# Kernel tuning notes

Measured on AMD Instinct MI355X. Metric: run time of the kernel, lower is better.

The kernel has to match this reference:

```python
import jax, jax.numpy as jnp
import numpy as np

QA = 4  # quaternion dimension (qa in the torch code)


def _bingham_sample(lam, key):
    """ACG rejection sampler for Bingham(lam), lam > 0, shape [N, 4].
    Faithful to bingham_rj: resample rejected rows until all accepted.
    Implemented with a fixed-shape lax.while_loop (resample everything,
    keep accepted rows via where) so it is jit-compatible."""
    sigacginv = 1.0 + 2.0 * lam            # [N,4]
    sig = jnp.sqrt(1.0 / sigacginv)        # SigACG, per-component std
    N = lam.shape[0]
    X0 = jnp.zeros((N, QA), lam.dtype)
    acc0 = jnp.zeros((N,), dtype=bool)

    half_qa = QA / 2.0
    log_qa = jnp.log(jnp.asarray(QA, lam.dtype))

    def cond(state):
        _, acc, _ = state
        return ~jnp.all(acc)

    def body(state):
        X, acc, key = state
        key, k1, k2 = jax.random.split(key, 3)
        yp = jax.random.normal(k1, (N, QA), lam.dtype) * sig
        y = yp / jnp.linalg.norm(yp, axis=1, keepdims=True)
        y2 = y * y
        lratio = (-jnp.sum(y2 * lam, axis=1)
                  - half_qa * log_qa
                  + 0.5 * (QA - 1)
                  + half_qa * jnp.log(jnp.sum(y2 * sigacginv, axis=1)))
        u = jax.random.uniform(k2, (N,), lam.dtype)
        # torch code: X[indx] = y (overwrite not-yet-accepted), then decide accept
        X = jnp.where(acc[:, None], X, y)
        acc = acc | (jnp.log(u) < lratio)
        return X, acc, key

    X, _, _ = jax.lax.while_loop(cond, body, (X0, acc0, key))
    return X


def _make_E(qn):
    """Build z_Q [N,4,4] from unit quaternions, exactly as reparameterize_rj."""
    q0, q1, q2, q3 = qn[:, 0], qn[:, 1], qn[:, 2], qn[:, 3]
    r1 = jnp.stack([q0, -q1, -q2, q3], axis=-1)
    r2 = jnp.stack([q1, q0, q3, q2], axis=-1)
    r3 = jnp.stack([q2, -q3, q0, -q1], axis=-1)
    r4 = jnp.stack([q3, q2, -q1, -q0], axis=-1)
    return jnp.stack([r1, r2, r3, r4], axis=1)  # rows stacked along dim 1


def setup_inputs() -> dict:
    key = jax.random.key(0)
    kq, kz = jax.random.split(key)
    N = 1048576
    q = jax.random.normal(kq, (N, 4), jnp.float32)
    # strictly negative, monotonically decreasing concentrations (Z0<Z1<Z2 in |.|)
    dZ = jax.random.uniform(kz, (N, 3), jnp.float32, minval=1e-3, maxval=100.0)
    Zbatch = -jnp.cumsum(dZ, axis=1)  # [N,3], all < 0
    return {"q": q, "Zbatch": Zbatch, "seed": 42}


def reference(q, Zbatch, seed):
    # F.normalize on the quaternion output (done in forward before reparameterize_rj)
    qn = q / jnp.linalg.norm(q, axis=1, keepdims=True)
    E = _make_E(qn)                                              # [N,4,4]
    N = q.shape[0]
    Zexp = jnp.concatenate(
        [jnp.full((N, 1), -1e-6, Zbatch.dtype), Zbatch], axis=1)  # [N,4], all < 0
    lam = -Zexp                                                   # lam > 0
    X = _bingham_sample(lam, jax.random.key(seed))                # [N,4]
    # torch.bmm(E.transpose(1,2), X.unsqueeze(2)).squeeze() == E^T @ x per row
    return jnp.einsum('nij,ni->nj', E, X)
```

## Files before the change

### kernel.cpp

```cpp
#include <hip/hip_runtime.h>
#include <cstdint>


#define DEVI __device__ __forceinline__
#define MAXT 96
#define GRID 512
#define NT 256
#define CMAX 2048
#define GANGA 56
#define NG 16
#define GW 4

DEVI uint32_t rotl32(uint32_t v, int s) { return (v << s) | (v >> (32 - s)); }

DEVI void tf2x32(uint32_t k0, uint32_t k1, uint32_t x0, uint32_t x1,
                 uint32_t& o0, uint32_t& o1) {
  const uint32_t kx = k0 ^ k1 ^ 0x1BD11BDAu;
  x0 += k0; x1 += k1;
#define TFR(r) x0 += x1; x1 = rotl32(x1, (r)); x1 ^= x0;
  TFR(13) TFR(15) TFR(26) TFR(6)
  x0 += k1; x1 += kx + 1u;
  TFR(17) TFR(29) TFR(16) TFR(24)
  x0 += kx; x1 += k0 + 2u;
  TFR(13) TFR(15) TFR(26) TFR(6)
  x0 += k0; x1 += k1 + 3u;
  TFR(17) TFR(29) TFR(16) TFR(24)
  x0 += k1; x1 += kx + 4u;
  TFR(13) TFR(15) TFR(26) TFR(6)
  x0 += kx; x1 += k0 + 5u;
#undef TFR
  o0 = x0; o1 = x1;
}

DEVI void tf_round5(uint32_t x0[5], uint32_t x1[5], int rr) {
#pragma unroll
  for (int j = 0; j < 5; ++j) {
    x0[j] += x1[j];
    x1[j] = rotl32(x1[j], rr);
    x1[j] ^= x0[j];
  }
}
DEVI void tf_inj5(uint32_t x0[5], uint32_t x1[5],
                  const uint32_t* sa, const uint32_t* sb, uint32_t add) {
#pragma unroll
  for (int j = 0; j < 5; ++j) { x0[j] += sa[j]; x1[j] += sb[j] + add; }
}

DEVI float u01_from_bits(uint32_t bits) {
  return __fsub_rn(__uint_as_float(0x3f800000u | (bits >> 9)), 1.0f);
}

DEVI void trial5(uint4 ck, uint32_t base, uint32_t ctr, float u[5]) {
  uint32_t s0[5], s1[5], s2k[5], x0[5], x1[5];
#pragma unroll
  for (int j = 0; j < 5; ++j) {
    uint32_t k0 = (j < 4) ? ck.x : ck.z;
    uint32_t k1 = (j < 4) ? ck.y : ck.w;
    s0[j] = k0; s1[j] = k1; s2k[j] = k0 ^ k1 ^ 0x1BD11BDAu;
    uint32_t c = (j < 4) ? (base + (uint32_t)j) : ctr;
    x0[j] = k0;
    x1[j] = c + k1;
  }
  tf_round5(x0, x1, 13); tf_round5(x0, x1, 15);
  tf_round5(x0, x1, 26); tf_round5(x0, x1, 6);
  tf_inj5(x0, x1, s1, s2k, 1u);
  tf_round5(x0, x1, 17); tf_round5(x0, x1, 29);
  tf_round5(x0, x1, 16); tf_round5(x0, x1, 24);
  tf_inj5(x0, x1, s2k, s0, 2u);
  tf_round5(x0, x1, 13); tf_round5(x0, x1, 15);
  tf_round5(x0, x1, 26); tf_round5(x0, x1, 6);
  tf_inj5(x0, x1, s0, s1, 3u);
  tf_round5(x0, x1, 17); tf_round5(x0, x1, 29);
  tf_round5(x0, x1, 16); tf_round5(x0, x1, 24);
  tf_inj5(x0, x1, s1, s2k, 4u);
  tf_round5(x0, x1, 13); tf_round5(x0, x1, 15);
  tf_round5(x0, x1, 26); tf_round5(x0, x1, 6);
  tf_inj5(x0, x1, s2k, s0, 5u);
#pragma unroll
  for (int j = 0; j < 5; ++j) u[j] = u01_from_bits(x0[j] ^ x1[j]);
}

template <int K>
DEVI void xla_logf_pos_k(const float* xf, float* out) {
  float e[K], m[K], z[K], y[K];
#pragma unroll
  for (int j = 0; j < K; ++j) {
    uint32_t bits = __float_as_uint(xf[j]);
    e[j] = (float)((int)(bits >> 23) - 126);
    m[j] = __uint_as_float((bits & 0x007fffffu) | 0x3f000000u);
    bool mc = m[j] < 0.70710678118654752440f;
    float e_lo = __fsub_rn(e[j], 1.0f);
    float m_lo = __fadd_rn(__fsub_rn(m[j], 1.0f), m[j]);
    float m_hi = __fsub_rn(m[j], 1.0f);
    e[j] = mc ? e_lo : e[j];
    m[j] = mc ? m_lo : m_hi;
    z[j] = __fmul_rn(m[j], m[j]);
    y[j] = 7.0376836292e-2f;
  }
  const float LC[8] = {-1.1514610310e-1f,  1.1676998740e-1f,
                       -1.2420140846e-1f,  1.4249322787e-1f,
                       -1.6668057665e-1f,  2.0000714765e-1f,
                       -2.4999993993e-1f,  3.3333331174e-1f};
#pragma unroll
  for (int s = 0; s < 8; ++s)
#pragma unroll
    for (int j = 0; j < K; ++j)
      y[j] = __fadd_rn(__fmul_rn(y[j], m[j]), LC[s]);
#pragma unroll
  for (int j = 0; j < K; ++j) {
    float t = __fmul_rn(__fmul_rn(y[j], m[j]), z[j]);
    t = __fadd_rn(t, __fmul_rn(e[j], -2.12194440e-4f));
    t = __fsub_rn(t, __fmul_rn(z[j], 0.5f));
    float r = __fadd_rn(m[j], t);
    out[j] = __fadd_rn(r, __fmul_rn(e[j], 0.693359375f));
  }
}

DEVI void xla_erfinv4_logu(const float* xin, float uu, float* res,
                           float& lg_uu) {
  float v[4], vp1[5], big[5], w[4], q[4], p[4];
  bool c[4];
#pragma unroll
  for (int j = 0; j < 4; ++j) {
    v[j] = -__fmul_rn(xin[j], xin[j]);
    vp1[j] = __fadd_rn(v[j], 1.0f);
  }
  vp1[4] = uu;
  xla_logf_pos_k<5>(vp1, big);
  lg_uu = big[4];
#pragma unroll
  for (int j = 0; j < 4; ++j) {
    float small = __fmul_rn(__fadd_rn(__fmul_rn(-0.5f, v[j]), 1.0f), v[j]);
    float l1p = (fabsf(v[j]) < 1e-4f) ? small : big[j];
    w[j] = -l1p;
    c[j] = (w[j] < 5.0f);
    float qc = __fsub_rn(w[j], 2.5f);
    float qr = __fsub_rn(sqrtf(w[j]), 3.0f);
    q[j] = c[j] ? qc : qr;
    p[j] = c[j] ? 2.81022636e-08f : -0.000200214257f;
  }
  const float CF[8] = { 3.43273939e-07f, -3.5233877e-06f, -4.39150654e-06f,
                        0.00021858087f,  -0.00125372503f, -0.00417768164f,
                        0.246640727f,     1.50140941f};
  const float CR[8] = { 0.000100950558f,  0.00134934322f, -0.00367342844f,
                        0.00573950773f,  -0.0076224613f,   0.00943887047f,
                        1.00167406f,      2.83297682f};
#pragma unroll
  for (int s = 0; s < 8; ++s)
#pragma unroll
    for (int j = 0; j < 4; ++j)
      p[j] = __fadd_rn(__fmul_rn(p[j], q[j]), c[j] ? CF[s] : CR[s]);
#pragma unroll
  for (int j = 0; j < 4; ++j) res[j] = __fmul_rn(p[j], xin[j]);
}

DEVI bool trial_eval(uint4 ck, int r,
                     float lam1, float lam2, float lam3,
                     float sgi1, float sgi2, float sgi3,
                     float sig1, float sig2, float sig3,
                     float sgi0, float sig0,
                     float& ry0, float& ry1, float& ry2, float& ry3) {
  const uint32_t base = ((uint32_t)r) * 4u;

  float u5[5];
  trial5(ck, base, (uint32_t)r, u5);
  float uu = u5[4];

  float xin[4];
#pragma unroll
  for (int j = 0; j < 4; ++j) {
    float x = __fadd_rn(__fmul_rn(u5[j], 2.0f), -0.99999994f);
    xin[j] = fmaxf(-0.99999994f, x);
  }
  float er[4], lg_uu;
  xla_erfinv4_logu(xin, uu, er, lg_uu);

  float y0 = __fmul_rn(__fmul_rn(1.41421356237309504880f, er[0]), sig0);
  float y1 = __fmul_rn(__fmul_rn(1.41421356237309504880f, er[1]), sig1);
  float y2v = __fmul_rn(__fmul_rn(1.41421356237309504880f, er[2]), sig2);
  float y3 = __fmul_rn(__fmul_rn(1.41421356237309504880f, er[3]), sig3);

  float n2 = __fmul_rn(y0, y0);
  n2 = __fadd_rn(n2, __fmul_rn(y1, y1));
  n2 = __fadd_rn(n2, __fmul_rn(y2v, y2v));
  n2 = __fadd_rn(n2, __fmul_rn(y3, y3));
  float nr = sqrtf(n2);
  y0 = __fdiv_rn(y0, nr); y1 = __fdiv_rn(y1, nr);
  y2v = __fdiv_rn(y2v, nr); y3 = __fdiv_rn(y3, nr);

  float s0q = __fmul_rn(y0, y0), s1q = __fmul_rn(y1, y1);
  float s2q = __fmul_rn(y2v, y2v), s3q = __fmul_rn(y3, y3);

  float s1v = __fmul_rn(s0q, 1e-6f);
  s1v = __fadd_rn(s1v, __fmul_rn(s1q, lam1));
  s1v = __fadd_rn(s1v, __fmul_rn(s2q, lam2));
  s1v = __fadd_rn(s1v, __fmul_rn(s3q, lam3));

  float s2v = __fmul_rn(s0q, sgi0);
  s2v = __fadd_rn(s2v, __fmul_rn(s1q, sgi1));
  s2v = __fadd_rn(s2v, __fmul_rn(s2q, sgi2));
  s2v = __fadd_rn(s2v, __fmul_rn(s3q, sgi3));

  float lg_s2[1];
  xla_logf_pos_k<1>(&s2v, lg_s2);

  float lr = __fsub_rn(-s1v, 2.7725887298583984f);
  lr = __fadd_rn(lr, 1.5f);
  lr = __fadd_rn(lr, __fmul_rn(2.0f, lg_s2[0]));

  float lu = (uu > 0.0f) ? lg_uu : -__builtin_inff();

  ry0 = y0; ry1 = y1; ry2 = y2v; ry3 = y3;
  return (lu < lr);
}

__global__ __launch_bounds__(256, 2) void campose_kernel(
    const float* __restrict__ q, const float* __restrict__ Z,
    float* __restrict__ out, const int* __restrict__ seedp, int N, int C) {
  __shared__ uint4 chain[MAXT + 1];
  __shared__ float rc[9][CMAX];
  __shared__ uint32_t next_row;
  __shared__ uint32_t wm;

  const int tid = threadIdx.x;
  const int lane = tid & 63;
  const int rbeg = blockIdx.x * C;
  const int rend = min(N, rbeg + C);
  const int crows = rend - rbeg;
  if (tid == 0) { next_row = (uint32_t)(rbeg + 192); wm = 0u; }

  for (int i = tid; i < crows; i += NT) {
    float z0 = Z[(size_t)(rbeg + i) * 3 + 0];
    float z1 = Z[(size_t)(rbeg + i) * 3 + 1];
    float z2 = Z[(size_t)(rbeg + i) * 3 + 2];
    float l1 = -z0, l2 = -z1, l3 = -z2;
    float g1 = __fadd_rn(1.0f, __fmul_rn(2.0f, l1));
    float g2 = __fadd_rn(1.0f, __fmul_rn(2.0f, l2));
    float g3 = __fadd_rn(1.0f, __fmul_rn(2.0f, l3));
    float s1_ = sqrtf(__fdiv_rn(1.0f, g1));
    float s2_ = sqrtf(__fdiv_rn(1.0f, g2));
    float s3_ = sqrtf(__fdiv_rn(1.0f, g3));
    rc[0][i] = g1; rc[1][i] = g2; rc[2][i] = g3;
    rc[3][i] = s1_; rc[4][i] = s2_; rc[5][i] = s3_;
    rc[6][i] = l1; rc[7][i] = l2; rc[8][i] = l3;
  }
  __syncthreads();

  const int wave = tid >> 6;
  if (wave == 0) {
    uint32_t ka = 0u, kb = (uint32_t)seedp[0];
    uint32_t x1i = (lane == 2) ? 0u : (uint32_t)(lane + 1);
    for (int t = 0; t < MAXT; ++t) {
      uint32_t o0 = 0u, o1 = 0u;
      if (lane < 3) tf2x32(ka, kb, 0u, x1i, o0, o1);
      uint32_t s1a = __shfl(o0, 0, 64), s1b = __shfl(o1, 0, 64);
      uint32_t s2a = __shfl(o0, 1, 64), s2b = __shfl(o1, 1, 64);
      if (lane == 0) chain[t] = make_uint4(s1a, s1b, s2a, s2b);
      ka = __shfl(o0, 2, 64); kb = __shfl(o1, 2, 64);
      __threadfence_block();
      if (lane == 0) *(volatile uint32_t*)&wm = (uint32_t)(t + 1);
    }
    if (lane == 0) chain[MAXT] = make_uint4(0u, 0u, 0u, 0u);
    __threadfence_block();
    if (lane == 0) *(volatile uint32_t*)&wm = (uint32_t)(MAXT + 1);
  }

  const float sgi0 = __fadd_rn(1.0f, __fmul_rn(2.0f, 1e-6f));
  const float sig0 = sqrtf(__fdiv_rn(1.0f, sgi0));

  int r, rn;
  if (wave == 0) {
    r  = (int)atomicAdd(&next_row, 1u);
    rn = (int)atomicAdd(&next_row, 1u);
  } else {
    r  = rbeg + (tid - 64);
    rn = (int)atomicAdd(&next_row, 1u);
  }
  bool have = (r < rend);
  float lam1 = 0, lam2 = 0, lam3 = 0;
  float sgi1 = 1, sgi2 = 1, sgi3 = 1;
  float sig1 = 1, sig2 = 1, sig3 = 1;
  if (have) {
    int li = r - rbeg;
    sgi1 = rc[0][li]; sgi2 = rc[1][li]; sgi3 = rc[2][li];
    sig1 = rc[3][li]; sig2 = rc[4][li]; sig3 = rc[5][li];
    lam1 = rc[6][li]; lam2 = rc[7][li]; lam3 = rc[8][li];
  }

  uint32_t wml = *(volatile uint32_t*)&wm;
  while (wml < 1u) wml = *(volatile uint32_t*)&wm;
  __threadfence_block();
  const uint4 ck0 = chain[0];
  uint4 ck = ck0;
  int t = 0;

  while (true) {
    uint64_t msk = __ballot(have);
    if (__popcll(msk) <= GANGA) break;
    if (have) {
      if (wml < (uint32_t)(t + 2)) {
        uint32_t w_ = *(volatile uint32_t*)&wm;
        while (w_ < (uint32_t)(t + 2)) w_ = *(volatile uint32_t*)&wm;
        __threadfence_block();
        wml = w_;
      }
      uint4 ckn = chain[t + 1];

      float y0, y1, y2v, y3;
      bool alr = trial_eval(ck, r, lam1, lam2, lam3, sgi1, sgi2, sgi3,
                            sig1, sig2, sig3, sgi0, sig0, y0, y1, y2v, y3);

      ++t;
      if (alr || (t >= MAXT)) {
        *reinterpret_cast<float4*>(out + (size_t)r * 4) =
            make_float4(y0, y1, y2v, y3);
        r = rn;
        int li = (r < rend ? r : rend - 1) - rbeg;
        sgi1 = rc[0][li]; sgi2 = rc[1][li]; sgi3 = rc[2][li];
        sig1 = rc[3][li]; sig2 = rc[4][li]; sig3 = rc[5][li];
        lam1 = rc[6][li]; lam2 = rc[7][li]; lam3 = rc[8][li];
        t = 0;
        ck = ck0;
        have = (r < rend);
        rn = (int)atomicAdd(&next_row, 1u);
      } else {
        ck = ckn;
      }
    }
  }

  uint64_t mask = __ballot(have);
  if (mask) {
    if (wml < (uint32_t)(MAXT + 1)) {
      uint32_t w_ = *(volatile uint32_t*)&wm;
      while (w_ < (uint32_t)(MAXT + 1)) w_ = *(volatile uint32_t*)&wm;
      __threadfence_block();
      wml = w_;
    }
    while (mask) {
      int G = __popcll(mask); if (G > NG) G = NG;
      const int g = lane >> 2, k = lane & 3;
      const bool gact = (g < G);
      const int gidx = gact ? g : 0;
      uint64_t m = mask;
      int sl = __ffsll((unsigned long long)m) - 1;
#pragma unroll
      for (int i = 1; i < NG; ++i) {
        m &= m - 1;
        int b = __ffsll((unsigned long long)m) - 1;
        sl = (i <= gidx && b >= 0) ? b : sl;
      }
      int rg = __shfl(r, sl, 64);
      int tg = __shfl(t, sl, 64);
      int li = rg - rbeg;
      float G1 = rc[0][li], G2 = rc[1][li], G3 = rc[2][li];
      float S1 = rc[3][li], S2 = rc[4][li], S3 = rc[5][li];
      float L1 = rc[6][li], L2 = rc[7][li], L3 = rc[8][li];
      int ts = tg + k;
      int tsc = ts < (MAXT - 1) ? ts : (MAXT - 1);
      uint4 cks = chain[tsc];
      float y0, y1, y2v, y3;
      bool alr = trial_eval(cks, rg, L1, L2, L3, G1, G2, G3,
                            S1, S2, S3, sgi0, sig0, y0, y1, y2v, y3);
      bool acc = alr || (ts >= MAXT - 1);
      uint64_t bal = __ballot(acc && gact);
      uint64_t gb = (bal >> (g * GW)) & 0xfull;
      int kwin = gb ? (__ffsll((unsigned long long)gb) - 1) : GW;
      if (gact && k == kwin) {
        *reinterpret_cast<float4*>(out + (size_t)rg * 4) =
            make_float4(y0, y1, y2v, y3);
      }
      int myidx = __popcll(mask & ((1ull << lane) - 1ull));
      if (have && myidx < G) {
        uint64_t gbb = (bal >> (myidx * GW)) & 0xfull;
        if (gbb) {
          r = rn;
          t = 0;
          have = (r < rend);
          rn = (int)atomicAdd(&next_row, 1u);
        } else {
          t += GW;
        }
      }
      mask = __ballot(have);
    }
  }

  __syncthreads();
  for (int i = rbeg + tid; i < rend; i += NT) {
    float4 yv = *reinterpret_cast<const float4*>(out + (size_t)i * 4);
    float4 qv = *reinterpret_cast<const float4*>(q + (size_t)i * 4);
    float a = qv.x, b = qv.y, c = qv.z, d = qv.w;
    float qn2 = __fmul_rn(a, a);
    qn2 = __fadd_rn(qn2, __fmul_rn(b, b));
    qn2 = __fadd_rn(qn2, __fmul_rn(c, c));
    qn2 = __fadd_rn(qn2, __fmul_rn(d, d));
    float qnr = sqrtf(qn2);
    a = __fdiv_rn(a, qnr); b = __fdiv_rn(b, qnr);
    c = __fdiv_rn(c, qnr); d = __fdiv_rn(d, qnr);
    float y0 = yv.x, y1 = yv.y, y2v = yv.z, y3 = yv.w;
    float o0v = __fadd_rn(__fadd_rn(__fadd_rn(__fmul_rn(a, y0), __fmul_rn(b, y1)),
                                    __fmul_rn(c, y2v)), __fmul_rn(d, y3));
    float o1v = __fadd_rn(__fadd_rn(__fadd_rn(__fmul_rn(-b, y0), __fmul_rn(a, y1)),
                                    __fmul_rn(-d, y2v)), __fmul_rn(c, y3));
    float o2v = __fadd_rn(__fadd_rn(__fadd_rn(__fmul_rn(-c, y0), __fmul_rn(d, y1)),
                                    __fmul_rn(a, y2v)), __fmul_rn(-b, y3));
    float o3v = __fadd_rn(__fadd_rn(__fadd_rn(__fmul_rn(d, y0), __fmul_rn(c, y1)),
                                    __fmul_rn(-b, y2v)), __fmul_rn(-a, y3));
    *reinterpret_cast<float4*>(out + (size_t)i * 4) =
        make_float4(o0v, o1v, o2v, o3v);
  }
}

extern "C" void kernel_launch(void* const* d_in, const int* in_sizes, int n_in,
                              void* d_out, int out_size, void* d_ws, size_t ws_size,
                              hipStream_t stream) {
  const float* q = (const float*)d_in[0];
  const float* Z = (const float*)d_in[1];
  const int* seed = (const int*)d_in[2];
  float* out = (float*)d_out;
  int N = in_sizes[0] / 4;

  int nb = GRID;
  int C = (N + nb - 1) / nb;
  if (C > CMAX) {
    nb = (N + CMAX - 1) / CMAX;
    C = (N + nb - 1) / nb;
  }
  campose_kernel<<<nb, NT, 0, stream>>>(q, Z, out, seed, N, C);
}
```

Measured before the change: 155.6 us.

## Use packed FP32 math in log/erfinv and narrow tail gangs to 2 lanes

```diff
diff --git a/kernel.cpp b/kernel.cpp
--- a/kernel.cpp
+++ b/kernel.cpp
@@ -7,9 +7,22 @@
 #define GRID 512
 #define NT 256
 #define CMAX 2048
-#define GANGA 56
-#define NG 16
-#define GW 4
+#define GANGA 62
+#define NG 32
+#define GW 2
+
+typedef float f32x2 __attribute__((ext_vector_type(2)));
+
+DEVI f32x2 pk_mul(f32x2 a, f32x2 b) {
+  f32x2 d;
+  asm("v_pk_mul_f32 %0, %1, %2" : "=v"(d) : "v"(a), "v"(b));
+  return d;
+}
+DEVI f32x2 pk_add(f32x2 a, f32x2 b) {
+  f32x2 d;
+  asm("v_pk_add_f32 %0, %1, %2" : "=v"(d) : "v"(a), "v"(b));
+  return d;
+}
 
 DEVI uint32_t rotl32(uint32_t v, int s) { return (v << s) | (v >> (32 - s)); }
 
@@ -116,9 +129,60 @@
   }
 }
 
+DEVI void xla_logf_pos5_pk(const float* xf, float* out) {
+  float e[5], m[5];
+#pragma unroll
+  for (int j = 0; j < 5; ++j) {
+    uint32_t bits = __float_as_uint(xf[j]);
+    e[j] = (float)((int)(bits >> 23) - 126);
+    m[j] = __uint_as_float((bits & 0x007fffffu) | 0x3f000000u);
+    bool mc = m[j] < 0.70710678118654752440f;
+    float e_lo = __fsub_rn(e[j], 1.0f);
+    float m_lo = __fadd_rn(__fsub_rn(m[j], 1.0f), m[j]);
+    float m_hi = __fsub_rn(m[j], 1.0f);
+    e[j] = mc ? e_lo : e[j];
+    m[j] = mc ? m_lo : m_hi;
+  }
+  f32x2 m01 = {m[0], m[1]}, m23 = {m[2], m[3]};
+  f32x2 z01 = pk_mul(m01, m01), z23 = pk_mul(m23, m23);
+  float z4 = __fmul_rn(m[4], m[4]);
+  f32x2 y01 = {7.0376836292e-2f, 7.0376836292e-2f};
+  f32x2 y23 = y01;
+  float y4 = 7.0376836292e-2f;
+  const float LC[8] = {-1.1514610310e-1f,  1.1676998740e-1f,
+                       -1.2420140846e-1f,  1.4249322787e-1f,
+                       -1.6668057665e-1f,  2.0000714765e-1f,
+                       -2.4999993993e-1f,  3.3333331174e-1f};
+#pragma unroll
+  for (int s = 0; s < 8; ++s) {
+    f32x2 lc2 = {LC[s], LC[s]};
+    y01 = pk_add(pk_mul(y01, m01), lc2);
+    y23 = pk_add(pk_mul(y23, m23), lc2);
+    y4 = __fadd_rn(__fmul_rn(y4, m[4]), LC[s]);
+  }
+  f32x2 e01 = {e[0], e[1]}, e23 = {e[2], e[3]};
+  const f32x2 c1 = {-2.12194440e-4f, -2.12194440e-4f};
+  const f32x2 nh = {-0.5f, -0.5f};
+  const f32x2 c2 = {0.693359375f, 0.693359375f};
+  f32x2 t01 = pk_mul(pk_mul(y01, m01), z01);
+  f32x2 t23 = pk_mul(pk_mul(y23, m23), z23);
+  t01 = pk_add(t01, pk_mul(e01, c1));
+  t23 = pk_add(t23, pk_mul(e23, c1));
+  t01 = pk_add(t01, pk_mul(z01, nh));
+  t23 = pk_add(t23, pk_mul(z23, nh));
+  f32x2 r01 = pk_add(m01, t01), r23 = pk_add(m23, t23);
+  r01 = pk_add(r01, pk_mul(e01, c2));
+  r23 = pk_add(r23, pk_mul(e23, c2));
+  out[0] = r01.x; out[1] = r01.y; out[2] = r23.x; out[3] = r23.y;
+  float t4 = __fmul_rn(__fmul_rn(y4, m[4]), z4);
+  t4 = __fadd_rn(t4, __fmul_rn(e[4], -2.12194440e-4f));
+  t4 = __fsub_rn(t4, __fmul_rn(z4, 0.5f));
+  out[4] = __fadd_rn(__fadd_rn(m[4], t4), __fmul_rn(e[4], 0.693359375f));
+}
+
 DEVI void xla_erfinv4_logu(const float* xin, float uu, float* res,
                            float& lg_uu) {
-  float v[4], vp1[5], big[5], w[4], q[4], p[4];
+  float v[4], vp1[5], big[5], w[4];
   bool c[4];
 #pragma unroll
   for (int j = 0; j < 4; ++j) {
@@ -126,7 +190,7 @@
     vp1[j] = __fadd_rn(v[j], 1.0f);
   }
   vp1[4] = uu;
-  xla_logf_pos_k<5>(vp1, big);
+  xla_logf_pos5_pk(vp1, big);
   lg_uu = big[4];
 #pragma unroll
   for (int j = 0; j < 4; ++j) {
@@ -134,10 +198,6 @@
     float l1p = (fabsf(v[j]) < 1e-4f) ? small : big[j];
     w[j] = -l1p;
     c[j] = (w[j] < 5.0f);
-    float qc = __fsub_rn(w[j], 2.5f);
-    float qr = __fsub_rn(sqrtf(w[j]), 3.0f);
-    q[j] = c[j] ? qc : qr;
-    p[j] = c[j] ? 2.81022636e-08f : -0.000200214257f;
   }
   const float CF[8] = { 3.43273939e-07f, -3.5233877e-06f, -4.39150654e-06f,
                         0.00021858087f,  -0.00125372503f, -0.00417768164f,
@@ -145,13 +205,39 @@
   const float CR[8] = { 0.000100950558f,  0.00134934322f, -0.00367342844f,
                         0.00573950773f,  -0.0076224613f,   0.00943887047f,
                         1.00167406f,      2.83297682f};
-#pragma unroll
-  for (int s = 0; s < 8; ++s)
-#pragma unroll
-    for (int j = 0; j < 4; ++j)
-      p[j] = __fadd_rn(__fmul_rn(p[j], q[j]), c[j] ? CF[s] : CR[s]);
-#pragma unroll
-  for (int j = 0; j < 4; ++j) res[j] = __fmul_rn(p[j], xin[j]);
+  bool slow = !(c[0] && c[1] && c[2] && c[3]);
+  if (__ballot(slow) == 0ull) {
+    f32x2 w01 = {w[0], w[1]}, w23 = {w[2], w[3]};
+    const f32x2 mt5 = {-2.5f, -2.5f};
+    f32x2 q01 = pk_add(w01, mt5), q23 = pk_add(w23, mt5);
+    f32x2 p01 = {2.81022636e-08f, 2.81022636e-08f};
+    f32x2 p23 = p01;
+#pragma unroll
+    for (int s = 0; s < 8; ++s) {
+      f32x2 cf2 = {CF[s], CF[s]};
+      p01 = pk_add(pk_mul(p01, q01), cf2);
+      p23 = pk_add(pk_mul(p23, q23), cf2);
+    }
+    f32x2 x01 = {xin[0], xin[1]}, x23 = {xin[2], xin[3]};
+    f32x2 r01 = pk_mul(p01, x01), r23 = pk_mul(p23, x23);
+    res[0] = r01.x; res[1] = r01.y; res[2] = r23.x; res[3] = r23.y;
+  } else {
+    float q[4], p[4];
+#pragma unroll
+    for (int j = 0; j < 4; ++j) {
+      float qc = __fsub_rn(w[j], 2.5f);
+      float qr = __fsub_rn(sqrtf(w[j]), 3.0f);
+      q[j] = c[j] ? qc : qr;
+      p[j] = c[j] ? 2.81022636e-08f : -0.000200214257f;
+    }
+#pragma unroll
+    for (int s = 0; s < 8; ++s)
+#pragma unroll
+      for (int j = 0; j < 4; ++j)
+        p[j] = __fadd_rn(__fmul_rn(p[j], q[j]), c[j] ? CF[s] : CR[s]);
+#pragma unroll
+    for (int j = 0; j < 4; ++j) res[j] = __fmul_rn(p[j], xin[j]);
+  }
 }
 
 DEVI bool trial_eval(uint4 ck, int r,
@@ -339,7 +425,7 @@
     }
     while (mask) {
       int G = __popcll(mask); if (G > NG) G = NG;
-      const int g = lane >> 2, k = lane & 3;
+      const int g = lane >> 1, k = lane & 1;
       const bool gact = (g < G);
       const int gidx = gact ? g : 0;
       uint64_t m = mask;
@@ -364,7 +450,7 @@
                             S1, S2, S3, sgi0, sig0, y0, y1, y2v, y3);
       bool acc = alr || (ts >= MAXT - 1);
       uint64_t bal = __ballot(acc && gact);
-      uint64_t gb = (bal >> (g * GW)) & 0xfull;
+      uint64_t gb = (bal >> (g * GW)) & 0x3ull;
       int kwin = gb ? (__ffsll((unsigned long long)gb) - 1) : GW;
       if (gact && k == kwin) {
         *reinterpret_cast<float4*>(out + (size_t)rg * 4) =
@@ -372,7 +458,7 @@
       }
       int myidx = __popcll(mask & ((1ull << lane) - 1ull));
       if (have && myidx < G) {
-        uint64_t gbb = (bal >> (myidx * GW)) & 0xfull;
+        uint64_t gbb = (bal >> (myidx * GW)) & 0x3ull;
         if (gbb) {
           r = rn;
           t = 0;
```

Result: slower. 172.7 us (+10.9%).
